# Kernel optimization log

Hardware: AMD Instinct MI355X
Metric: run time of the kernel (lower is better)

The kernel has to match this reference:

```python
import jax, jax.numpy as jnp
import numpy as np

K = 3
HALF = K // 2  # original code uses python2-style k/2 integer division
NUM_CLASSES = 201
IDENTITY = jnp.array([1.0, 0.0, 0.0, 0.0, 1.0, 0.0], dtype=jnp.float32)

def conv2d(x, w, b, pad):
    y = jax.lax.conv_general_dilated(x, w, (1, 1), [(pad, pad), (pad, pad)],
                                     dimension_numbers=('NCHW', 'OIHW', 'NCHW'))
    return y if b is None else y + b[None, :, None, None]

def affine_grid(theta, k):
    # F.affine_grid, align_corners=True (old-torch default matching the /(H-1) normalization)
    base = jnp.linspace(-1.0, 1.0, k, dtype=theta.dtype)
    xb = base[None, None, :]  # varies along width
    yb = base[None, :, None]  # varies along height
    gx = theta[:, 0, 0, None, None] * xb + theta[:, 0, 1, None, None] * yb + theta[:, 0, 2, None, None]
    gy = theta[:, 1, 0, None, None] * xb + theta[:, 1, 1, None, None] * yb + theta[:, 1, 2, None, None]
    return jnp.stack([gx, gy], axis=-1)  # [N, k, k, 2]

def make_aux(grid, B, S, H, W):
    # per-location absolute sampling coords, renormalized to [-1,1] over the full map
    off = HALF + jnp.arange(S, dtype=grid.dtype)
    gx = (grid[..., 0] * HALF).reshape(B, S, S, K, K) + off[None, :, None, None, None]
    gy = (grid[..., 1] * HALF).reshape(B, S, S, K, K) + off[None, None, :, None, None]
    auxx = gx.reshape(-1, K, K) / (H - 1) * 2.0 - 1.0
    auxy = gy.reshape(-1, K, K) / (W - 1) * 2.0 - 1.0
    return auxx, auxy

def grid_sample(x, grid, bidx):
    # bilinear, align_corners=True, zero padding; avoids materializing tile(x,0,S*S)
    B, C, H, W = x.shape
    gx = (grid[..., 0] + 1.0) * 0.5 * (W - 1)
    gy = (grid[..., 1] + 1.0) * 0.5 * (H - 1)
    x0 = jnp.floor(gx); y0 = jnp.floor(gy)
    wx1 = gx - x0; wy1 = gy - y0
    def gather(yi, xi):
        valid = (yi >= 0) & (yi <= H - 1) & (xi >= 0) & (xi <= W - 1)
        yc = jnp.clip(yi, 0, H - 1).astype(jnp.int32)
        xc = jnp.clip(xi, 0, W - 1).astype(jnp.int32)
        v = x[bidx[:, None, None], :, yc, xc]  # [N, k, k, C]
        return v * valid[..., None]
    out = (gather(y0, x0) * ((1 - wy1) * (1 - wx1))[..., None]
         + gather(y0, x0 + 1) * ((1 - wy1) * wx1)[..., None]
         + gather(y0 + 1, x0) * (wy1 * (1 - wx1))[..., None]
         + gather(y0 + 1, x0 + 1) * (wy1 * wx1)[..., None])
    return jnp.transpose(out, (0, 3, 1, 2))  # [N, C, k, k]

def compute_scores(x, p, check):
    B, C, H, W = x.shape
    h = jax.nn.relu(conv2d(x, p['stn0_w'], p['stn0_b'], HALF))
    out = conv2d(h, p['stn1_w'], None, 0) * (1.0 - check) + IDENTITY[None, :, None, None]
    S = out.shape[2]  # square maps assumed (required by original view logic)
    theta = jnp.transpose(out, (0, 3, 2, 1)).reshape(-1, 2, 3)  # flatten order (b, w, h)
    grid = affine_grid(theta, K)
    auxx, auxy = make_aux(grid, B, S, H, W)
    auxgrid = jnp.stack([auxx, auxy], axis=3)
    bidx = jnp.repeat(jnp.arange(B), S * S)
    xs = grid_sample(x, auxgrid, bidx)  # [B*S*S, C, K, K]
    feat = xs.reshape(xs.shape[0], -1) @ p['conv_w'].T + p['conv_b']
    output = jnp.transpose(feat.reshape(B, S, S, -1), (0, 3, 2, 1))
    output = jnp.einsum('bfhw,of->bohw', jax.nn.relu(output), p['last_w']) + p['last_b'][None, :, None, None]
    return output, theta, auxx, auxy, S

def box_from_aux(auxx, auxy, dl, conf, image_dim):
    tx = ((auxx + 1.0) * 0.5).reshape(auxx.shape[0], -1)[dl]
    ty = ((auxy + 1.0) * 0.5).reshape(auxy.shape[0], -1)[dl]
    lo, hi = 0.0, image_dim - 1
    return jnp.stack([jnp.clip(tx.min(1) * image_dim, lo, hi),
                      jnp.clip(ty.min(1) * image_dim, lo, hi),
                      jnp.clip(tx.max(1) * image_dim, lo, hi),
                      jnp.clip(ty.max(1) * image_dim, lo, hi),
                      conf], axis=1)

def max_boxes(l, pred, S, auxx, auxy, image_dim):
    B = l.shape[0]
    scores = l[jnp.arange(B), pred]          # [B, S*S]
    dl0 = jnp.argmax(scores, axis=1)
    conf = jnp.max(scores, axis=1)
    dl = (dl0 % S) * S + dl0 // S + jnp.arange(B) * (S * S)  # swap (h,w)->(w,h) flat index
    return box_from_aux(auxx, auxy, dl, conf, image_dim), dl, conf

def nt_aux(B, S, H, W):
    grid0 = affine_grid(IDENTITY.reshape(1, 2, 3), K)
    grid = jnp.broadcast_to(grid0, (B * S * S, K, K, 2))
    return make_aux(grid, B, S, H, W)

def _forward(x0, x1, p, check, image_dim):
    B = x0.shape[0]
    s5, th5, ax5, ay5, S5 = compute_scores(x0, p, check)
    s4, th4, ax4, ay4, S4 = compute_scores(x1, p, check)
    theta_diff = jnp.concatenate([IDENTITY.reshape(1, 2, 3) - th5,
                                  IDENTITY.reshape(1, 2, 3) - th4], axis=0)
    sc5 = s5.reshape(B, NUM_CLASSES, -1)
    sc4 = s4.reshape(B, NUM_CLASSES, -1)
    score = jnp.concatenate([sc5, sc4], axis=2)
    joint = jax.nn.softmax(score.reshape(B, -1), axis=1).reshape(B, NUM_CLASSES, -1)
    likelihood = joint.sum(2)
    L5 = sc5.shape[2]
    l5 = joint[:, :, :L5]
    l4 = joint[:, :, L5:]
    pred = jnp.argmax(likelihood, axis=1)
    sg = jax.lax.stop_gradient  # torch.no_grad block
    box5, dl5, conf5 = max_boxes(sg(l5), pred, S5, sg(ax5), sg(ay5), image_dim)
    ntx5, nty5 = nt_aux(B, S5, x0.shape[2], x0.shape[3])
    boxNT5 = box_from_aux(ntx5, nty5, dl5, conf5, image_dim)
    box4, dl4, conf4 = max_boxes(sg(l4), pred, S4, sg(ax4), sg(ay4), image_dim)
    ntx4, nty4 = nt_aux(B, S4, x1.shape[2], x1.shape[3])
    boxNT4 = box_from_aux(ntx4, nty4, dl4, conf4, image_dim)
    boxes = jnp.stack([box5, box4], axis=1)       # [B, 2, 5]
    boxes_NT = jnp.stack([boxNT5, boxNT4], axis=1)
    mi = jnp.argmax(boxes[:, :, 4], axis=1)
    boxes = boxes[jnp.arange(B), mi]
    boxes_NT = boxes_NT[jnp.arange(B), mi]
    max_l5 = jnp.max(l5[jnp.arange(B), pred], axis=1)
    max_l4 = jnp.max(l4[jnp.arange(B), pred], axis=1)
    reg_score = jnp.sum(jnp.maximum(0.0, max_l4 - max_l5))
    return likelihood, boxes, boxes_NT, theta_diff, reg_score

def setup_inputs() -> dict:
    key = jax.random.key(0)
    ks = jax.random.split(key, 10)
    B, C, F = 32, 256, 1024
    x0 = jax.random.normal(ks[0], (B, C, 10, 10), jnp.float32)
    x1 = jax.random.normal(ks[1], (B, C, 20, 20), jnp.float32)
    stn0_w = jax.random.normal(ks[2], (C, C, 3, 3), jnp.float32) * 0.02
    stn0_b = jax.random.normal(ks[3], (C,), jnp.float32) * 0.01
    stn1_w = jax.random.normal(ks[4], (6, C, 3, 3), jnp.float32) * 0.01
    conv_w = jax.random.normal(ks[5], (F, C * K * K), jnp.float32) * 0.02
    conv_b = jax.random.normal(ks[6], (F,), jnp.float32) * 0.01
    last_w = jax.random.normal(ks[7], (NUM_CLASSES, F), jnp.float32) * 0.03
    last_b = jax.random.normal(ks[8], (NUM_CLASSES,), jnp.float32) * 0.01
    return {'x0': x0, 'x1': x1, 'stn0_w': stn0_w, 'stn0_b': stn0_b, 'stn1_w': stn1_w,
            'conv_w': conv_w, 'conv_b': conv_b, 'last_w': last_w, 'last_b': last_b,
            'check': 0, 'image_dim': 320}

def reference(x0, x1, stn0_w, stn0_b, stn1_w, conv_w, conv_b, last_w, last_b, check, image_dim):
    p = {'stn0_w': stn0_w, 'stn0_b': stn0_b, 'stn1_w': stn1_w,
         'conv_w': conv_w, 'conv_b': conv_b, 'last_w': last_w, 'last_b': last_b}
    return _forward(x0, x1, p, float(check), image_dim)
```

## Files before the change

kernel.cpp:

```cpp
#include <hip/hip_runtime.h>
#include <cmath>

#define TPB 256
#define TPB2 512

constexpr int Bb = 32, Cc = 256, Ff = 1024, Oo = 201;
constexpr int H0 = 10, S0 = 8,  N0 = Bb * S0 * S0;
constexpr int H1 = 20, S1 = 18, N1 = Bb * S1 * S1;
constexpr int NT_ALL = N0 + N1;
constexpr int KC = Cc * 9;
constexpr int KP = Cc * 16;
constexpr int L5 = S0 * S0, L4 = S1 * S1, LT = L5 + L4;
constexpr int CHMAX = 4224;
constexpr int M1 = Bb * H0 * H0;
constexpr int MCONV = M1 + Bb * H1 * H1;

constexpr size_t SZ_CW  = (size_t)Ff * KC;
constexpr size_t SZ_W0P = (size_t)Cc * KP;
constexpr size_t SZ_LWP = (size_t)256 * Ff;

constexpr size_t B_CWH = 0;
constexpr size_t B_CWL = B_CWH + SZ_CW * 2;
constexpr size_t B_GXY = B_CWL + SZ_CW * 2;
constexpr size_t B_LWH = B_GXY + (size_t)NT_ALL * 18 * 4;
constexpr size_t B_LWL = B_LWH + SZ_LWP * 2;
constexpr size_t B_SC  = B_LWL + SZ_LWP * 2;
constexpr size_t B_XSH = B_SC + (size_t)Bb * Oo * LT * 4;
constexpr size_t B_XSL = B_XSH + (size_t)CHMAX * KC * 2;
constexpr size_t B_FCH = B_XSL + (size_t)CHMAX * KC * 2;
constexpr size_t B_FCL = B_FCH + (size_t)CHMAX * Ff * 2;
constexpr size_t B_MX  = B_FCL + (size_t)CHMAX * Ff * 2;
constexpr size_t B_SM  = B_MX + 128;
constexpr size_t B_RP  = B_SM + 128;
constexpr size_t B_END = B_RP + 128;
constexpr size_t B_W0H = B_XSH;
constexpr size_t B_W0L = B_XSH + SZ_W0P * 2;
constexpr size_t B_H0  = B_XSL;
constexpr size_t B_H1  = B_XSL + (size_t)Bb * Cc * H0 * H0 * 4;
constexpr size_t B_C2  = B_FCH;

constexpr size_t O_LIK = 0;
constexpr size_t O_BOX = O_LIK + Bb * Oo;
constexpr size_t O_NT  = O_BOX + Bb * 5;
constexpr size_t O_TD  = O_NT + Bb * 5;
constexpr size_t O_REG = O_TD + (size_t)NT_ALL * 6;

typedef __attribute__((ext_vector_type(8))) short bf16x8;
typedef __attribute__((ext_vector_type(4))) float f32x4;

__device__ __forceinline__ void tsplit(float v, short& h, short& l) {
    unsigned u = __builtin_bit_cast(unsigned, v);
    h = (short)(u >> 16);
    float hf = __builtin_bit_cast(float, u & 0xffff0000u);
    float r = v - hf;
    l = (short)(__builtin_bit_cast(unsigned, r) >> 16);
}
__device__ __forceinline__ float clampf(float x, float lo, float hi) {
    return fminf(fmaxf(x, lo), hi);
}
__device__ __forceinline__ void gload16(const void* g, void* l) {
    __builtin_amdgcn_global_load_lds(
        (const __attribute__((address_space(1))) void*)g,
        (__attribute__((address_space(3))) void*)l, 16, 0, 0);
}
__device__ __forceinline__ size_t aidx(int row, int k, int KD) {
    return ((size_t)(row >> 7) * (KD >> 5) + (k >> 5)) * 4096
         + (size_t)(((row & 127) >> 4) * 512 + ((k >> 3) & 3) * 128 + (row & 15) * 8 + (k & 7));
}

__global__ __launch_bounds__(TPB)
void splitp_k(const float* __restrict__ src, short* __restrict__ hi,
              short* __restrict__ lo, int nrows)
{
    int idx = blockIdx.x * TPB + threadIdx.x;
    if (idx >= nrows * 288) return;
    int row = idx / 288, r = idx - row * 288;
    int t = r >> 5, cg = r & 31;
    const float* sp = src + (size_t)row * KC + (size_t)cg * 8 * 9 + t;
    bf16x8 hv, lv;
    #pragma unroll
    for (int e = 0; e < 8; e++) {
        short h, l; tsplit(sp[e * 9], h, l);
        hv[e] = h; lv[e] = l;
    }
    size_t dst = aidx(row, t * 256 + cg * 8, KC);
    *(bf16x8*)&hi[dst] = hv;
    *(bf16x8*)&lo[dst] = lv;
}

__global__ __launch_bounds__(TPB)
void splitp16_k(const float* __restrict__ src, short* __restrict__ hi,
                short* __restrict__ lo, int nrows)
{
    int idx = blockIdx.x * TPB + threadIdx.x;
    if (idx >= nrows * KP) return;
    int row = idx >> 12, kq = idx & (KP - 1);
    int c = kq >> 4, t = kq & 15;
    float v = (t < 9) ? src[(size_t)row * KC + c * 9 + t] : 0.f;
    short h, l; tsplit(v, h, l);
    hi[idx] = h; lo[idx] = l;
}

__global__ __launch_bounds__(TPB)
void splitlw_k(const float* __restrict__ src, short* __restrict__ hi,
               short* __restrict__ lo)
{
    int idx = blockIdx.x * TPB + threadIdx.x;
    if (idx >= (int)SZ_LWP) return;
    int row = idx >> 10, k = idx & 1023;
    float v = (row < Oo) ? src[idx] : 0.f;
    short h, l; tsplit(v, h, l);
    size_t dst = aidx(row, k, Ff);
    hi[dst] = h; lo[dst] = l;
}

__global__ __launch_bounds__(TPB)
void mat_k(const float* __restrict__ x0, const float* __restrict__ x1,
           const float* __restrict__ gxy, short* __restrict__ xsH,
           short* __restrict__ xsL, int base, int rows)
{
    int idx = blockIdx.x * TPB + threadIdx.x;
    if (idx >= rows * 288) return;
    int mloc = idx / 288, r = idx - mloc * 288;
    int j = r >> 5, cg = r & 31;
    int m = base + mloc;
    const float* xp; int H, loc, SS;
    if (m < N0) { xp = x0; H = H0; loc = m; SS = 64; }
    else        { xp = x1; H = H1; loc = m - N0; SS = 324; }
    int b = loc / SS;
    float gx = gxy[(size_t)m * 18 + j];
    float gy = gxy[(size_t)m * 18 + 9 + j];
    float xf = floorf(gx), yf = floorf(gy);
    float wx = gx - xf, wy = gy - yf;
    int ix = (int)xf, iy = (int)yf;
    int cx0 = min(max(ix, 0), H - 1), cy0 = min(max(iy, 0), H - 1);
    bool vx0 = (ix >= 0 && ix < H), vx1 = (ix >= -1 && ix < H - 1);
    bool vy0 = (iy >= 0 && iy < H), vy1 = (iy >= -1 && iy < H - 1);
    float wxL = vx0 ? (1.f - wx) : (vx1 ? wx : 0.f);
    float wxR = (vx0 && vx1) ? wx : 0.f;
    float wyT = vy0 ? (1.f - wy) : (vy1 ? wy : 0.f);
    float wyB = (vy0 && vy1) ? wy : 0.f;
    float wTL = wyT * wxL, wTR = wyT * wxR, wBL = wyB * wxL, wBR = wyB * wxR;
    int o   = cy0 * H + cx0;
    int oTR = (wTR != 0.f) ? o + 1     : o;
    int oBL = (wBL != 0.f) ? o + H     : o;
    int oBR = (wBR != 0.f) ? o + H + 1 : o;
    const float* cp = xp + ((size_t)b * Cc + cg * 8) * (H * H);
    bf16x8 hv, lv;
    #pragma unroll
    for (int e = 0; e < 8; e++) {
        float v = cp[o] * wTL + cp[oTR] * wTR + cp[oBL] * wBL + cp[oBR] * wBR;
        short h, l; tsplit(v, h, l); hv[e] = h; lv[e] = l;
        cp += H * H;
    }
    size_t dst = aidx(mloc, j * 256 + cg * 8, KC);
    *(bf16x8*)&xsH[dst] = hv;
    *(bf16x8*)&xsL[dst] = lv;
}

template<int KD>
__global__ __launch_bounds__(TPB2, 4)
void mgemm(const float* __restrict__ x0s, const float* __restrict__ x1s,
           const short* __restrict__ Bh, const short* __restrict__ Bl,
           const float* __restrict__ bias,
           float* __restrict__ outF, float* __restrict__ outF2)
{
    __shared__ short As[2][4][128][8];
    __shared__ short Bs[2][4][64][8];
    __shared__ float slab[1600];

    const int tid = threadIdx.x;
    const int lane = tid & 63;
    const int wid = tid >> 6;
    const int wm = (wid >> 2) * 64, wn = (wid & 3) * 16;
    const int ml = tid & 127;
    const int cc = (tid >> 7) & 1;
    const int half = tid >> 8;
    const int bm = blockIdx.y * 128, bn = blockIdx.x * 64;

    f32x4 acc[4];
    #pragma unroll
    for (int i = 0; i < 4; i++) acc[i] = (f32x4){0.f, 0.f, 0.f, 0.f};

    const float* xsrc = nullptr;
    int Hh = 0, PLSZr = 0, UPPr = 0, bat0 = 0, batidx = 0, nu = 0;
    float wvt[9]; int offt[9];
    {
        int lbase;
        if (bm < M1) { xsrc = x0s; Hh = H0; lbase = bm; }
        else         { xsrc = x1s; Hh = H1; lbase = bm - M1; }
        PLSZr = Hh * Hh; UPPr = PLSZr >> 2;
        int mGl = lbase + ml;
        int bA = mGl / PLSZr; int rem = mGl - bA * PLSZr;
        int yA = rem / Hh, xA = rem - (rem / Hh) * Hh;
        bat0 = lbase / PLSZr;
        int nb = (lbase + 127) / PLSZr - bat0 + 1;
        batidx = bA - bat0;
        nu = nb * 2 * UPPr;
        #pragma unroll
        for (int t = 0; t < 9; t++) {
            int ky = t / 3 - 1, kx = t - (t / 3) * 3 - 1;
            int yy = yA + ky, xx = xA + kx;
            bool ok = (yy >= 0 && yy < Hh && xx >= 0 && xx < Hh);
            offt[t] = ok ? (yy * Hh + xx) : 0;
            wvt[t] = ok ? 1.f : 0.f;
        }
    }

    float4 rv0 = {}, rv1 = {};
    float4 pv0 = {}, pv1 = {};
    auto issue_loads = [&](int kb, float4& a0, float4& a1) {
        const int c0 = kb >> 4;
        #pragma unroll
        for (int q = 0; q < 2; q++) {
            int i = tid + q * TPB2;
            if (i < nu) {
                int pl = i / UPPr, u = i - pl * UPPr;
                int bi = pl >> 1, ccq = pl & 1;
                float4 v = *(const float4*)(xsrc +
                    ((size_t)(bat0 + bi) * Cc + c0 + ccq) * PLSZr + u * 4);
                if (q == 0) a0 = v; else a1 = v;
            }
        }
    };
    auto write_slab = [&](const float4& a0, const float4& a1) {
        #pragma unroll
        for (int q = 0; q < 2; q++) {
            int i = tid + q * TPB2;
            if (i < nu)
                *(float4*)&slab[i * 4] = (q == 0) ? a0 : a1;
        }
    };

    issue_loads(0, rv0, rv1);

    for (int kb = 0; kb < KD; kb += 32) {
        write_slab(rv0, rv1);
        if (kb + 32 < KD) issue_loads(kb + 32, pv0, pv1);
        __syncthreads();
        {
            int hilo = wid & 1, kg = wid >> 1;
            const short* g = (hilo ? Bl : Bh) + (size_t)(bn + lane) * KD + kb + kg * 8;
            gload16(g, &Bs[hilo][kg][0][0]);
        }
        {
            const float* sp = &slab[(batidx * 2 + cc) * PLSZr];
            if (half == 0) {
                bf16x8 hv, lv;
                #pragma unroll
                for (int e = 0; e < 8; e++) {
                    float v = sp[offt[e]] * wvt[e];
                    short h, l; tsplit(v, h, l); hv[e] = h; lv[e] = l;
                }
                *(bf16x8*)&As[0][cc * 2][ml][0] = hv;
                *(bf16x8*)&As[1][cc * 2][ml][0] = lv;
            } else {
                bf16x8 hv2 = {}, lv2 = {};
                float v = sp[offt[8]] * wvt[8];
                short h, l; tsplit(v, h, l); hv2[0] = h; lv2[0] = l;
                *(bf16x8*)&As[0][cc * 2 + 1][ml][0] = hv2;
                *(bf16x8*)&As[1][cc * 2 + 1][ml][0] = lv2;
            }
        }
        __syncthreads();
        {
            const int kq = lane >> 4, r = lane & 15;
            bf16x8 ah[4], al[4];
            #pragma unroll
            for (int i = 0; i < 4; i++) {
                ah[i] = *(const bf16x8*)&As[0][kq][wm + i * 16 + r][0];
                al[i] = *(const bf16x8*)&As[1][kq][wm + i * 16 + r][0];
            }
            bf16x8 bh = *(const bf16x8*)&Bs[0][kq][wn + r][0];
            bf16x8 bl = *(const bf16x8*)&Bs[1][kq][wn + r][0];
            #pragma unroll
            for (int i = 0; i < 4; i++) {
                acc[i] = __builtin_amdgcn_mfma_f32_16x16x32_bf16(ah[i], bh, acc[i], 0, 0, 0);
                acc[i] = __builtin_amdgcn_mfma_f32_16x16x32_bf16(al[i], bh, acc[i], 0, 0, 0);
                acc[i] = __builtin_amdgcn_mfma_f32_16x16x32_bf16(ah[i], bl, acc[i], 0, 0, 0);
            }
        }
        rv0 = pv0; rv1 = pv1;
    }

    const int kq = lane >> 4, rr = lane & 15;
    #pragma unroll
    for (int i = 0; i < 4; i++) {
        #pragma unroll
        for (int r = 0; r < 4; r++) {
            const int gm = bm + wm + i * 16 + kq * 4 + r;
            const int gn = bn + wn + rr;
            float v = acc[i][r];
            float* hp; int Hq, lr;
            if (gm < M1) { hp = outF; Hq = H0; lr = gm; }
            else         { hp = outF2; Hq = H1; lr = gm - M1; }
            int PL = Hq * Hq;
            int bq = lr / PL; int rem = lr - bq * PL;
            int yq = rem / Hq; int xq = rem - yq * Hq;
            hp[((size_t)bq * Cc + gn) * PL + yq * Hq + xq] = fmaxf(v + bias[gn], 0.f);
        }
    }
}

template<int MODE, int KD>
__global__ __launch_bounds__(TPB, 3)
void mgemm4(const short* __restrict__ AsH_, const short* __restrict__ AsL_,
            const short* __restrict__ Bh, const short* __restrict__ Bl,
            const float* __restrict__ bias,
            float* __restrict__ outF, short* __restrict__ outH,
            short* __restrict__ outL, int base)
{
    constexpr int NSTEP = KD / 32;
    const int tid = threadIdx.x;
    const int lane = tid & 63;
    const int wid = tid >> 6;
    const int wm = (wid >> 1) * 64, wn = (wid & 1) * 32;
    const int bm = blockIdx.y * 128, bn = blockIdx.x * 64;

    const size_t ablk0 = (size_t)(bm >> 7) * NSTEP * 4096;
    const size_t bblk0 = (size_t)(bn >> 7) * NSTEP * 4096;
    const int ai = wm >> 4;
    const int bi = ((bn & 64) + wn) >> 4;
    const int lo8 = lane * 8;

    f32x4 acc[4][2];
    #pragma unroll
    for (int i = 0; i < 4; i++)
        #pragma unroll
        for (int j = 0; j < 2; j++)
            acc[i][j] = (f32x4){0.f, 0.f, 0.f, 0.f};

    bf16x8 Ah[2][4], Al[2][4], Bhf[2][2], Blf[2][2];

    auto LOAD = [&](int s, int t) {
        const size_t ab = ablk0 + (size_t)t * 4096;
        const size_t bb = bblk0 + (size_t)t * 4096;
        #pragma unroll
        for (int i = 0; i < 4; i++) {
            Ah[s][i] = *(const bf16x8*)(AsH_ + ab + (ai + i) * 512 + lo8);
            Al[s][i] = *(const bf16x8*)(AsL_ + ab + (ai + i) * 512 + lo8);
        }
        #pragma unroll
        for (int j = 0; j < 2; j++) {
            Bhf[s][j] = *(const bf16x8*)(Bh + bb + (bi + j) * 512 + lo8);
            Blf[s][j] = *(const bf16x8*)(Bl + bb + (bi + j) * 512 + lo8);
        }
    };
    auto MM = [&](int s) {
        #pragma unroll
        for (int i = 0; i < 4; i++)
            #pragma unroll
            for (int j = 0; j < 2; j++) {
                acc[i][j] = __builtin_amdgcn_mfma_f32_16x16x32_bf16(Ah[s][i], Bhf[s][j], acc[i][j], 0, 0, 0);
                acc[i][j] = __builtin_amdgcn_mfma_f32_16x16x32_bf16(Al[s][i], Bhf[s][j], acc[i][j], 0, 0, 0);
                acc[i][j] = __builtin_amdgcn_mfma_f32_16x16x32_bf16(Ah[s][i], Blf[s][j], acc[i][j], 0, 0, 0);
            }
    };

    LOAD(0, 0);
    for (int t = 0; t < NSTEP; t += 2) {
        LOAD(1, t + 1);
        MM(0);
        if (t + 2 < NSTEP) LOAD(0, t + 2);
        MM(1);
    }

    const int kq = lane >> 4, rr = lane & 15;
    #pragma unroll
    for (int i = 0; i < 4; i++) {
        #pragma unroll
        for (int r = 0; r < 4; r++) {
            const int gm = bm + wm + i * 16 + kq * 4 + r;
            #pragma unroll
            for (int j = 0; j < 2; j++) {
                const int gn = bn + wn + j * 16 + rr;
                float v = acc[i][j][r];
                if constexpr (MODE == 4) {
                    float q = fmaxf(v + bias[gn], 0.f);
                    short h, l; tsplit(q, h, l);
                    size_t d = aidx(gm, gn, Ff);
                    outH[d] = h;
                    outL[d] = l;
                } else {
                    if (gn < Oo) {
                        int g = base + gm;
                        int bq, pos;
                        if (g < N0) {
                            int lo = g & 63; bq = g >> 6;
                            pos = (lo & 7) * 8 + (lo >> 3);
                        } else {
                            int gg = g - N0; bq = gg / 324; int lo = gg - bq * 324;
                            int xq = lo / 18, yq = lo - xq * 18;
                            pos = L5 + yq * 18 + xq;
                        }
                        outF[((size_t)bq * Oo + gn) * LT + pos] = v + bias[gn];
                    }
                }
            }
        }
    }
}

__global__ __launch_bounds__(TPB)
void conv2_k(const float* __restrict__ h0, const float* __restrict__ h1,
             const float* __restrict__ w1, float* __restrict__ c2)
{
    __shared__ float wl[6][KC];
    __shared__ float part[8][32][6];
    const int tid = threadIdx.x;
    for (int i = tid; i < 6 * KC; i += TPB) wl[i / KC][i - (i / KC) * KC] = w1[i];
    __syncthreads();
    const int row = blockIdx.x * 32 + (tid & 31);
    const int cig = tid >> 5;
    const float* hsrc; int H, S, loc;
    if (row < N0) { hsrc = h0; H = H0; S = S0; loc = row; }
    else          { hsrc = h1; H = H1; S = S1; loc = row - N0; }
    int SS = S * S;
    int b = loc / SS; int rem = loc - b * SS;
    int xq = rem / S; int yq = rem - xq * S;
    float acc[6] = {};
    for (int ci = cig * 32; ci < cig * 32 + 32; ci++) {
        const float* hp = hsrc + ((size_t)(b * Cc + ci) * H + yq) * H + xq;
        #pragma unroll
        for (int ky = 0; ky < 3; ky++)
            #pragma unroll
            for (int kx = 0; kx < 3; kx++) {
                float a = hp[ky * H + kx];
                int kk = ci * 9 + ky * 3 + kx;
                #pragma unroll
                for (int n = 0; n < 6; n++) acc[n] = fmaf(a, wl[n][kk], acc[n]);
            }
    }
    #pragma unroll
    for (int n = 0; n < 6; n++) part[cig][tid & 31][n] = acc[n];
    __syncthreads();
    if (cig == 0) {
        #pragma unroll
        for (int n = 0; n < 6; n++) {
            float s = 0.f;
            for (int g = 0; g < 8; g++) s += part[g][tid & 31][n];
            c2[(size_t)row * 6 + n] = s;
        }
    }
}

__global__ __launch_bounds__(TPB)
void theta_aux_k(const float* __restrict__ c2, const int* __restrict__ checkp,
                 float* __restrict__ td, float* __restrict__ gxy)
{
    int n = blockIdx.x * TPB + threadIdx.x;
    if (n >= NT_ALL) return;
    float omc = 1.0f - (float)checkp[0];
    const float I[6] = {1.f, 0.f, 0.f, 0.f, 1.f, 0.f};
    float th[6];
    #pragma unroll
    for (int i = 0; i < 6; i++) {
        float v = c2[(size_t)n * 6 + i] * omc + I[i];
        th[i] = v;
        td[(size_t)n * 6 + i] = I[i] - v;
    }
    int S, loc;
    if (n < N0) { S = S0; loc = n; } else { S = S1; loc = n - N0; }
    int SS = S * S;
    int rem = loc % SS;
    int xx = rem / S, yy = rem % S;
    #pragma unroll
    for (int ky = 0; ky < 3; ky++)
        #pragma unroll
        for (int kx = 0; kx < 3; kx++) {
            float bx = (float)(kx - 1), by = (float)(ky - 1);
            gxy[(size_t)n * 18 + ky * 3 + kx]     = th[0] * bx + th[1] * by + th[2] + 1.0f + (float)xx;
            gxy[(size_t)n * 18 + 9 + ky * 3 + kx] = th[3] * bx + th[4] * by + th[5] + 1.0f + (float)yy;
        }
}

__global__ __launch_bounds__(TPB)
void statslik_k(const float* __restrict__ sc, float* __restrict__ mx,
                float* __restrict__ sm, float* __restrict__ lik)
{
    int b = blockIdx.x, tid = threadIdx.x;
    const float* p = sc + (size_t)b * Oo * LT;
    constexpr int PER = Oo * LT;
    __shared__ float red[TPB];
    float m = -3.4e38f;
    for (int i = tid; i < PER; i += TPB) m = fmaxf(m, p[i]);
    red[tid] = m;
    for (int off = 128; off; off >>= 1) { __syncthreads(); if (tid < off) red[tid] = fmaxf(red[tid], red[tid + off]); }
    __syncthreads();
    m = red[0];
    __syncthreads();
    float so = 0.f;
    if (tid < Oo) {
        const float* q = p + (size_t)tid * LT;
        for (int i = 0; i < LT; i++) so += expf(q[i] - m);
    }
    red[tid] = so;
    for (int off = 128; off; off >>= 1) { __syncthreads(); if (tid < off) red[tid] += red[tid + off]; }
    __syncthreads();
    float smt = red[0];
    if (tid < Oo) lik[b * Oo + tid] = so / smt;
    if (tid == 0) { mx[b] = m; sm[b] = smt; }
}

__global__ __launch_bounds__(TPB)
void box_k(const float* __restrict__ sc, const float* __restrict__ lik,
           const float* __restrict__ mx, const float* __restrict__ sm,
           const float* __restrict__ gxy, const int* __restrict__ imdp,
           float* __restrict__ boxes, float* __restrict__ boxesNT,
           float* __restrict__ regpart)
{
    int b = blockIdx.x, tid = threadIdx.x;
    __shared__ float sv[TPB];
    __shared__ int si[TPB];

    float v = (tid < Oo) ? lik[b * Oo + tid] : -3.4e38f;
    sv[tid] = v; si[tid] = tid;
    for (int off = 128; off; off >>= 1) {
        __syncthreads();
        if (tid < off) {
            float v2 = sv[tid + off]; int i2 = si[tid + off];
            if (v2 > sv[tid] || (v2 == sv[tid] && i2 < si[tid])) { sv[tid] = v2; si[tid] = i2; }
        }
    }
    __syncthreads();
    int pred = si[0];
    __syncthreads();

    const float* p = sc + ((size_t)b * Oo + pred) * LT;
    float b5 = -3.4e38f; int i5 = 1 << 30;
    float b4 = -3.4e38f; int i4 = 1 << 30;
    for (int pos = tid; pos < LT; pos += TPB) {
        float s = p[pos];
        if (pos < L5) { if (s > b5) { b5 = s; i5 = pos; } }
        else { int q = pos - L5; if (s > b4) { b4 = s; i4 = q; } }
    }
    sv[tid] = b5; si[tid] = i5;
    for (int off = 128; off; off >>= 1) {
        __syncthreads();
        if (tid < off) {
            float v2 = sv[tid + off]; int i2 = si[tid + off];
            if (v2 > sv[tid] || (v2 == sv[tid] && i2 < si[tid])) { sv[tid] = v2; si[tid] = i2; }
        }
    }
    __syncthreads();
    float m5 = sv[0]; int d5 = si[0];
    __syncthreads();
    sv[tid] = b4; si[tid] = i4;
    for (int off = 128; off; off >>= 1) {
        __syncthreads();
        if (tid < off) {
            float v2 = sv[tid + off]; int i2 = si[tid + off];
            if (v2 > sv[tid] || (v2 == sv[tid] && i2 < si[tid])) { sv[tid] = v2; si[tid] = i2; }
        }
    }
    __syncthreads();
    float m4 = sv[0]; int d4 = si[0];

    if (tid == 0) {
        float m = mx[b], s = sm[b];
        float conf5 = expf(m5 - m) / s;
        float conf4 = expf(m4 - m) / s;
        float imd = (float)imdp[0];
        float lo = 0.f, hi = imd - 1.f;

        int xx5 = d5 % S0, yy5 = d5 / S0;
        int n5 = b * (S0 * S0) + xx5 * S0 + yy5;
        const float* g = gxy + (size_t)n5 * 18;
        float txm = 1e30f, txM = -1e30f, tym = 1e30f, tyM = -1e30f;
        for (int j = 0; j < 9; j++) {
            float tx = g[j] / 9.f, ty = g[9 + j] / 9.f;
            txm = fminf(txm, tx); txM = fmaxf(txM, tx);
            tym = fminf(tym, ty); tyM = fmaxf(tyM, ty);
        }
        float box5[5] = { clampf(txm * imd, lo, hi), clampf(tym * imd, lo, hi),
                          clampf(txM * imd, lo, hi), clampf(tyM * imd, lo, hi), conf5 };
        float nt5[5]  = { clampf((float)xx5 / 9.f * imd, lo, hi), clampf((float)yy5 / 9.f * imd, lo, hi),
                          clampf((float)(xx5 + 2) / 9.f * imd, lo, hi), clampf((float)(yy5 + 2) / 9.f * imd, lo, hi), conf5 };

        int xx4 = d4 % S1, yy4 = d4 / S1;
        int n4 = N0 + b * (S1 * S1) + xx4 * S1 + yy4;
        const float* g4 = gxy + (size_t)n4 * 18;
        float txm4 = 1e30f, txM4 = -1e30f, tym4 = 1e30f, tyM4 = -1e30f;
        for (int j = 0; j < 9; j++) {
            float tx = g4[j] / 19.f, ty = g4[9 + j] / 19.f;
            txm4 = fminf(txm4, tx); txM4 = fmaxf(txM4, tx);
            tym4 = fminf(tym4, ty); tyM4 = fmaxf(tyM4, ty);
        }
        float box4[5] = { clampf(txm4 * imd, lo, hi), clampf(tym4 * imd, lo, hi),
                          clampf(txM4 * imd, lo, hi), clampf(tyM4 * imd, lo, hi), conf4 };
        float nt4[5]  = { clampf((float)xx4 / 19.f * imd, lo, hi), clampf((float)yy4 / 19.f * imd, lo, hi),
                          clampf((float)(xx4 + 2) / 19.f * imd, lo, hi), clampf((float)(yy4 + 2) / 19.f * imd, lo, hi), conf4 };

        int mi = (conf4 > conf5) ? 1 : 0;
        for (int i = 0; i < 5; i++) {
            boxes[b * 5 + i]   = mi ? box4[i] : box5[i];
            boxesNT[b * 5 + i] = mi ? nt4[i] : nt5[i];
        }
        regpart[b] = fmaxf(conf4 - conf5, 0.f);
    }
}

__global__ void reg_k(const float* __restrict__ regpart, float* __restrict__ outreg)
{
    if (threadIdx.x == 0) {
        float s = 0.f;
        for (int b = 0; b < Bb; b++) s += regpart[b];
        outreg[0] = s;
    }
}

__global__ void sentinel_k(float* out, int n)
{
    int i = blockIdx.x * 256 + threadIdx.x;
    if (i < n) out[i] = 12345.0f;
}

extern "C" void kernel_launch(void* const* d_in, const int* in_sizes, int n_in,
                              void* d_out, int out_size, void* d_ws, size_t ws_size,
                              hipStream_t stream)
{
    const float* x0 = (const float*)d_in[0];
    const float* x1 = (const float*)d_in[1];
    const float* w0 = (const float*)d_in[2];
    const float* b0 = (const float*)d_in[3];
    const float* w1 = (const float*)d_in[4];
    const float* cw = (const float*)d_in[5];
    const float* cb = (const float*)d_in[6];
    const float* lw = (const float*)d_in[7];
    const float* lb = (const float*)d_in[8];
    const int* checkp = (const int*)d_in[9];
    const int* imdp   = (const int*)d_in[10];

    if (ws_size < B_END) {
        sentinel_k<<<dim3((out_size + 255) / 256), dim3(256), 0, stream>>>((float*)d_out, out_size);
        return;
    }

    char* wsb = (char*)d_ws;
    short* cwh = (short*)(wsb + B_CWH);
    short* cwl = (short*)(wsb + B_CWL);
    float* gxy = (float*)(wsb + B_GXY);
    short* lwh = (short*)(wsb + B_LWH);
    short* lwl = (short*)(wsb + B_LWL);
    float* sc  = (float*)(wsb + B_SC);
    short* xsH = (short*)(wsb + B_XSH);
    short* xsL = (short*)(wsb + B_XSL);
    short* fcH = (short*)(wsb + B_FCH);
    short* fcL = (short*)(wsb + B_FCL);
    float* mx  = (float*)(wsb + B_MX);
    float* sm  = (float*)(wsb + B_SM);
    float* rp  = (float*)(wsb + B_RP);
    short* w0h = (short*)(wsb + B_W0H);
    short* w0l = (short*)(wsb + B_W0L);
    float* h0  = (float*)(wsb + B_H0);
    float* h1  = (float*)(wsb + B_H1);
    float* c2  = (float*)(wsb + B_C2);

    float* out   = (float*)d_out;
    float* o_lik = out + O_LIK;
    float* o_box = out + O_BOX;
    float* o_nt  = out + O_NT;
    float* o_td  = out + O_TD;
    float* o_reg = out + O_REG;

    dim3 blk(TPB);

    splitp_k  <<<dim3((Ff * 288 + TPB - 1) / TPB), blk, 0, stream>>>(cw, cwh, cwl, Ff);
    splitp16_k<<<dim3((int)((SZ_W0P + TPB - 1) / TPB)), blk, 0, stream>>>(w0, w0h, w0l, Cc);
    splitlw_k <<<dim3((int)((SZ_LWP + TPB - 1) / TPB)), blk, 0, stream>>>(lw, lwh, lwl);

    mgemm<KP><<<dim3(4, MCONV / 128), dim3(TPB2), 0, stream>>>(
        x0, x1, w0h, w0l, b0, h0, h1);

    conv2_k<<<dim3(NT_ALL / 32), blk, 0, stream>>>(h0, h1, w1, c2);

    theta_aux_k<<<dim3((NT_ALL + TPB - 1) / TPB), blk, 0, stream>>>(c2, checkp, o_td, gxy);

    const int bases[3] = {0, 4096, 8192};
    const int sizes[3] = {4096, 4096, 4224};
    for (int c = 0; c < 3; c++) {
        int basei = bases[c], rows = sizes[c];
        int mt = rows / 128;
        mat_k<<<dim3((rows * 288 + TPB - 1) / TPB), blk, 0, stream>>>(
            x0, x1, gxy, xsH, xsL, basei, rows);
        mgemm4<4, KC><<<dim3(16, mt), blk, 0, stream>>>(
            xsH, xsL, cwh, cwl, cb, nullptr, fcH, fcL, 0);
        mgemm4<5, Ff><<<dim3(4, mt), blk, 0, stream>>>(
            fcH, fcL, lwh, lwl, lb, sc, nullptr, nullptr, basei);
    }

    statslik_k<<<dim3(Bb), blk, 0, stream>>>(sc, mx, sm, o_lik);
    box_k<<<dim3(Bb), blk, 0, stream>>>(sc, o_lik, mx, sm, gxy, imdp, o_box, o_nt, rp);
    reg_k<<<dim3(1), dim3(64), 0, stream>>>(rp, o_reg);
}
```

Before: 864.3 us.

## Double K-step in implicit-im2col conv GEMM and fuse stats with box kernel

The mgemm conv kernel now processes 64 K-elements (four input channels) per iteration instead of 32. That halves the number of barrier-separated iterations and doubles the shared-memory A/B tiles and the input slab, and every thread now builds both the 8-tap and the 1-tap fragments. Separately, the softmax-stats/likelihood kernel and the box kernel are merged into one launch, so max and sum stay in registers and skip a workspace round trip. The larger shared-memory footprint may lower occupancy.

```diff
diff --git a/kernel.cpp b/kernel.cpp
--- a/kernel.cpp
+++ b/kernel.cpp
@@ -29,10 +29,8 @@
 constexpr size_t B_XSL = B_XSH + (size_t)CHMAX * KC * 2;
 constexpr size_t B_FCH = B_XSL + (size_t)CHMAX * KC * 2;
 constexpr size_t B_FCL = B_FCH + (size_t)CHMAX * Ff * 2;
-constexpr size_t B_MX  = B_FCL + (size_t)CHMAX * Ff * 2;
-constexpr size_t B_SM  = B_MX + 128;
-constexpr size_t B_RP  = B_SM + 128;
-constexpr size_t B_END = B_RP + 128;
+constexpr size_t B_RP  = B_FCL + (size_t)CHMAX * Ff * 2;
+constexpr size_t B_END = B_RP + 256;
 constexpr size_t B_W0H = B_XSH;
 constexpr size_t B_W0L = B_XSH + SZ_W0P * 2;
 constexpr size_t B_H0  = B_XSL;
@@ -165,17 +163,16 @@
            const float* __restrict__ bias,
            float* __restrict__ outF, float* __restrict__ outF2)
 {
-    __shared__ short As[2][4][128][8];
-    __shared__ short Bs[2][4][64][8];
-    __shared__ float slab[1600];
+    __shared__ short As[2][8][128][8];
+    __shared__ short Bs[2][8][64][8];
+    __shared__ float slab[3200];
 
     const int tid = threadIdx.x;
     const int lane = tid & 63;
     const int wid = tid >> 6;
     const int wm = (wid >> 2) * 64, wn = (wid & 3) * 16;
     const int ml = tid & 127;
-    const int cc = (tid >> 7) & 1;
-    const int half = tid >> 8;
+    const int sl0 = tid >> 7;
     const int bm = blockIdx.y * 128, bn = blockIdx.x * 64;
 
     f32x4 acc[4];
@@ -196,7 +193,7 @@
         bat0 = lbase / PLSZr;
         int nb = (lbase + 127) / PLSZr - bat0 + 1;
         batidx = bA - bat0;
-        nu = nb * 2 * UPPr;
+        nu = nb * 4 * UPPr;
         #pragma unroll
         for (int t = 0; t < 9; t++) {
             int ky = t / 3 - 1, kx = t - (t / 3) * 3 - 1;
@@ -216,7 +213,7 @@
             int i = tid + q * TPB2;
             if (i < nu) {
                 int pl = i / UPPr, u = i - pl * UPPr;
-                int bi = pl >> 1, ccq = pl & 1;
+                int bi = pl >> 2, ccq = pl & 3;
                 float4 v = *(const float4*)(xsrc +
                     ((size_t)(bat0 + bi) * Cc + c0 + ccq) * PLSZr + u * 4);
                 if (q == 0) a0 = v; else a1 = v;
@@ -234,50 +231,52 @@
 
     issue_loads(0, rv0, rv1);
 
-    for (int kb = 0; kb < KD; kb += 32) {
+    for (int kb = 0; kb < KD; kb += 64) {
         write_slab(rv0, rv1);
-        if (kb + 32 < KD) issue_loads(kb + 32, pv0, pv1);
+        if (kb + 64 < KD) issue_loads(kb + 64, pv0, pv1);
         __syncthreads();
         {
-            int hilo = wid & 1, kg = wid >> 1;
-            const short* g = (hilo ? Bl : Bh) + (size_t)(bn + lane) * KD + kb + kg * 8;
-            gload16(g, &Bs[hilo][kg][0][0]);
+            int hilo = wid & 1, s0 = wid >> 1;
+            const short* gB = (hilo ? Bl : Bh) + (size_t)(bn + lane) * KD + kb;
+            gload16(gB + s0 * 8,       &Bs[hilo][s0][0][0]);
+            gload16(gB + (s0 + 4) * 8, &Bs[hilo][s0 + 4][0][0]);
         }
         {
-            const float* sp = &slab[(batidx * 2 + cc) * PLSZr];
-            if (half == 0) {
-                bf16x8 hv, lv;
-                #pragma unroll
-                for (int e = 0; e < 8; e++) {
-                    float v = sp[offt[e]] * wvt[e];
-                    short h, l; tsplit(v, h, l); hv[e] = h; lv[e] = l;
-                }
-                *(bf16x8*)&As[0][cc * 2][ml][0] = hv;
-                *(bf16x8*)&As[1][cc * 2][ml][0] = lv;
-            } else {
-                bf16x8 hv2 = {}, lv2 = {};
-                float v = sp[offt[8]] * wvt[8];
-                short h, l; tsplit(v, h, l); hv2[0] = h; lv2[0] = l;
-                *(bf16x8*)&As[0][cc * 2 + 1][ml][0] = hv2;
-                *(bf16x8*)&As[1][cc * 2 + 1][ml][0] = lv2;
+            const float* sp = &slab[(batidx * 4 + sl0) * PLSZr];
+            bf16x8 hv, lv;
+            #pragma unroll
+            for (int e = 0; e < 8; e++) {
+                float v = sp[offt[e]] * wvt[e];
+                short h, l; tsplit(v, h, l); hv[e] = h; lv[e] = l;
             }
+            *(bf16x8*)&As[0][sl0 * 2][ml][0] = hv;
+            *(bf16x8*)&As[1][sl0 * 2][ml][0] = lv;
+            bf16x8 hv2 = {}, lv2 = {};
+            { float v = sp[offt[8]] * wvt[8];
+              short h, l; tsplit(v, h, l); hv2[0] = h; lv2[0] = l; }
+            *(bf16x8*)&As[0][sl0 * 2 + 1][ml][0] = hv2;
+            *(bf16x8*)&As[1][sl0 * 2 + 1][ml][0] = lv2;
         }
         __syncthreads();
         {
             const int kq = lane >> 4, r = lane & 15;
-            bf16x8 ah[4], al[4];
             #pragma unroll
-            for (int i = 0; i < 4; i++) {
-                ah[i] = *(const bf16x8*)&As[0][kq][wm + i * 16 + r][0];
-                al[i] = *(const bf16x8*)&As[1][kq][wm + i * 16 + r][0];
-            }
-            bf16x8 bh = *(const bf16x8*)&Bs[0][kq][wn + r][0];
-            bf16x8 bl = *(const bf16x8*)&Bs[1][kq][wn + r][0];
-            #pragma unroll
-            for (int i = 0; i < 4; i++) {
-                acc[i] = __builtin_amdgcn_mfma_f32_16x16x32_bf16(ah[i], bh, acc[i], 0, 0, 0);
-                acc[i] = __builtin_amdgcn_mfma_f32_16x16x32_bf16(al[i], bh, acc[i], 0, 0, 0);
-                acc[i] = __builtin_amdgcn_mfma_f32_16x16x32_bf16(ah[i], bl, acc[i], 0, 0, 0);
+            for (int kh = 0; kh < 2; kh++) {
+                const int kgf = kh * 4 + kq;
+                bf16x8 ah[4], al[4];
+                #pragma unroll
+                for (int i = 0; i < 4; i++) {
+                    ah[i] = *(const bf16x8*)&As[0][kgf][wm + i * 16 + r][0];
+                    al[i] = *(const bf16x8*)&As[1][kgf][wm + i * 16 + r][0];
+                }
+                bf16x8 bh = *(const bf16x8*)&Bs[0][kgf][wn + r][0];
+                bf16x8 bl = *(const bf16x8*)&Bs[1][kgf][wn + r][0];
+                #pragma unroll
+                for (int i = 0; i < 4; i++) {
+                    acc[i] = __builtin_amdgcn_mfma_f32_16x16x32_bf16(ah[i], bh, acc[i], 0, 0, 0);
+                    acc[i] = __builtin_amdgcn_mfma_f32_16x16x32_bf16(al[i], bh, acc[i], 0, 0, 0);
+                    acc[i] = __builtin_amdgcn_mfma_f32_16x16x32_bf16(ah[i], bl, acc[i], 0, 0, 0);
+                }
             }
         }
         rv0 = pv0; rv1 = pv1;
@@ -475,13 +474,17 @@
 }
 
 __global__ __launch_bounds__(TPB)
-void statslik_k(const float* __restrict__ sc, float* __restrict__ mx,
-                float* __restrict__ sm, float* __restrict__ lik)
+void statsbox_k(const float* __restrict__ sc, const float* __restrict__ gxy,
+                const int* __restrict__ imdp, float* __restrict__ lik,
+                float* __restrict__ boxes, float* __restrict__ boxesNT,
+                float* __restrict__ regpart)
 {
     int b = blockIdx.x, tid = threadIdx.x;
     const float* p = sc + (size_t)b * Oo * LT;
     constexpr int PER = Oo * LT;
     __shared__ float red[TPB];
+    __shared__ int redi[TPB];
+
     float m = -3.4e38f;
     for (int i = tid; i < PER; i += TPB) m = fmaxf(m, p[i]);
     red[tid] = m;
@@ -489,6 +492,7 @@
     __syncthreads();
     m = red[0];
     __syncthreads();
+
     float so = 0.f;
     if (tid < Oo) {
         const float* q = p + (size_t)tid * LT;
@@ -498,68 +502,55 @@
     for (int off = 128; off; off >>= 1) { __syncthreads(); if (tid < off) red[tid] += red[tid + off]; }
     __syncthreads();
     float smt = red[0];
-    if (tid < Oo) lik[b * Oo + tid] = so / smt;
-    if (tid == 0) { mx[b] = m; sm[b] = smt; }
-}
-
-__global__ __launch_bounds__(TPB)
-void box_k(const float* __restrict__ sc, const float* __restrict__ lik,
-           const float* __restrict__ mx, const float* __restrict__ sm,
-           const float* __restrict__ gxy, const int* __restrict__ imdp,
-           float* __restrict__ boxes, float* __restrict__ boxesNT,
-           float* __restrict__ regpart)
-{
-    int b = blockIdx.x, tid = threadIdx.x;
-    __shared__ float sv[TPB];
-    __shared__ int si[TPB];
-
-    float v = (tid < Oo) ? lik[b * Oo + tid] : -3.4e38f;
-    sv[tid] = v; si[tid] = tid;
+    float mylik = (tid < Oo) ? so / smt : -3.4e38f;
+    if (tid < Oo) lik[b * Oo + tid] = mylik;
+    __syncthreads();
+
+    red[tid] = mylik; redi[tid] = tid;
     for (int off = 128; off; off >>= 1) {
         __syncthreads();
         if (tid < off) {
-            float v2 = sv[tid + off]; int i2 = si[tid + off];
-            if (v2 > sv[tid] || (v2 == sv[tid] && i2 < si[tid])) { sv[tid] = v2; si[tid] = i2; }
-        }
-    }
-    __syncthreads();
-    int pred = si[0];
-    __syncthreads();
-
-    const float* p = sc + ((size_t)b * Oo + pred) * LT;
+            float v2 = red[tid + off]; int i2 = redi[tid + off];
+            if (v2 > red[tid] || (v2 == red[tid] && i2 < redi[tid])) { red[tid] = v2; redi[tid] = i2; }
+        }
+    }
+    __syncthreads();
+    int pred = redi[0];
+    __syncthreads();
+
+    const float* pr = p + (size_t)pred * LT;
     float b5 = -3.4e38f; int i5 = 1 << 30;
     float b4 = -3.4e38f; int i4 = 1 << 30;
     for (int pos = tid; pos < LT; pos += TPB) {
-        float s = p[pos];
+        float s = pr[pos];
         if (pos < L5) { if (s > b5) { b5 = s; i5 = pos; } }
         else { int q = pos - L5; if (s > b4) { b4 = s; i4 = q; } }
     }
-    sv[tid] = b5; si[tid] = i5;
+    red[tid] = b5; redi[tid] = i5;
     for (int off = 128; off; off >>= 1) {
         __syncthreads();
         if (tid < off) {
-            float v2 = sv[tid + off]; int i2 = si[tid + off];
-            if (v2 > sv[tid] || (v2 == sv[tid] && i2 < si[tid])) { sv[tid] = v2; si[tid] = i2; }
-        }
-    }
-    __syncthreads();
-    float m5 = sv[0]; int d5 = si[0];
-    __syncthreads();
-    sv[tid] = b4; si[tid] = i4;
+            float v2 = red[tid + off]; int i2 = redi[tid + off];
+            if (v2 > red[tid] || (v2 == red[tid] && i2 < redi[tid])) { red[tid] = v2; redi[tid] = i2; }
+        }
+    }
+    __syncthreads();
+    float m5 = red[0]; int d5 = redi[0];
+    __syncthreads();
+    red[tid] = b4; redi[tid] = i4;
     for (int off = 128; off; off >>= 1) {
         __syncthreads();
         if (tid < off) {
-            float v2 = sv[tid + off]; int i2 = si[tid + off];
-            if (v2 > sv[tid] || (v2 == sv[tid] && i2 < si[tid])) { sv[tid] = v2; si[tid] = i2; }
-        }
-    }
-    __syncthreads();
-    float m4 = sv[0]; int d4 = si[0];
+            float v2 = red[tid + off]; int i2 = redi[tid + off];
+            if (v2 > red[tid] || (v2 == red[tid] && i2 < redi[tid])) { red[tid] = v2; redi[tid] = i2; }
+        }
+    }
+    __syncthreads();
+    float m4 = red[0]; int d4 = redi[0];
 
     if (tid == 0) {
-        float m = mx[b], s = sm[b];
-        float conf5 = expf(m5 - m) / s;
-        float conf4 = expf(m4 - m) / s;
+        float conf5 = expf(m5 - m) / smt;
+        float conf4 = expf(m4 - m) / smt;
         float imd = (float)imdp[0];
         float lo = 0.f, hi = imd - 1.f;
 
@@ -647,8 +638,6 @@
     short* xsL = (short*)(wsb + B_XSL);
     short* fcH = (short*)(wsb + B_FCH);
     short* fcL = (short*)(wsb + B_FCL);
-    float* mx  = (float*)(wsb + B_MX);
-    float* sm  = (float*)(wsb + B_SM);
     float* rp  = (float*)(wsb + B_RP);
     short* w0h = (short*)(wsb + B_W0H);
     short* w0l = (short*)(wsb + B_W0L);
@@ -689,7 +678,6 @@
             fcH, fcL, lwh, lwl, lb, sc, nullptr, nullptr, basei);
     }
 
-    statslik_k<<<dim3(Bb), blk, 0, stream>>>(sc, mx, sm, o_lik);
-    box_k<<<dim3(Bb), blk, 0, stream>>>(sc, o_lik, mx, sm, gxy, imdp, o_box, o_nt, rp);
+    statsbox_k<<<dim3(Bb), blk, 0, stream>>>(sc, gxy, imdp, o_lik, o_box, o_nt, rp);
     reg_k<<<dim3(1), dim3(64), 0, stream>>>(rp, o_reg);
 }
```

Result: no change. 856.1 us (median of 2 runs) (-0.9%).
